# Kernel optimization log

Measured on AMD Instinct MI355X. Metric: run time of the kernel, lower is better.

Reference implementation:

```python
import jax, jax.numpy as jnp
import numpy as np

NUM_LABELS = 1000
HIDDEN = 512
BATCH = 65536
NOISE_STD = 0.1
L_STAB, L_CENTER, L_SEP, L_BRIER = 1.0, 0.1, 0.01, 1.0


def setup_inputs() -> dict:
    key = jax.random.key(0)
    k1, k2, k3, k4, k5 = jax.random.split(key, 5)
    cls_rep = jax.random.normal(k1, (BATCH, HIDDEN), dtype=jnp.float32)
    logits = jax.random.normal(k2, (BATCH, NUM_LABELS), dtype=jnp.float32)
    labels = jax.random.randint(k3, (BATCH,), 0, NUM_LABELS)
    W = jax.random.normal(k4, (HIDDEN, NUM_LABELS), dtype=jnp.float32) * 0.02
    b = jnp.zeros((NUM_LABELS,), dtype=jnp.float32)
    noise = jax.random.normal(k5, (BATCH, HIDDEN), dtype=jnp.float32)
    centers = jnp.zeros((NUM_LABELS, HIDDEN), dtype=jnp.float32)
    return {"cls_rep": cls_rep, "logits": logits, "labels": labels,
            "W": W, "b": b, "noise": noise, "centers": centers}


def _compute_all(cls_rep, logits, labels, W, b, noise, centers):
    # --- update_centers (init branch, no_grad): per-class mean via segment_sum ---
    ones = jnp.ones((cls_rep.shape[0],), dtype=cls_rep.dtype)
    counts = jax.ops.segment_sum(ones, labels, num_segments=NUM_LABELS)           # [C]
    sums = jax.ops.segment_sum(cls_rep, labels, num_segments=NUM_LABELS)          # [C, H]
    present = counts > 0
    batch_means = sums / jnp.maximum(counts, 1.0)[:, None]
    new_centers = jnp.where(present[:, None], batch_means, centers)               # [C, H]
    new_centers = jax.lax.stop_gradient(new_centers)

    # --- stability: classifier(cls_rep + noise_std * eps) vs clean logits ---
    logits_noisy = (cls_rep + NOISE_STD * noise) @ W + b                          # [B, C]
    stab = jnp.mean((logits_noisy - logits) ** 2)

    # --- center loss: gather centroids, MSE ---
    center = jnp.mean((cls_rep - new_centers[labels]) ** 2)

    # --- separation: cdist + exp, minus exp(0)*num_labels ---
    sq = jnp.sum(new_centers ** 2, axis=1)                                        # [C]
    d2 = jnp.maximum(sq[:, None] + sq[None, :] - 2.0 * new_centers @ new_centers.T, 0.0)
    dist = jnp.sqrt(d2)                                                           # [C, C]
    I = jnp.eye(NUM_LABELS, dtype=dist.dtype)
    sep = jnp.sum(jnp.exp(-dist + I)) - jnp.float32(NUM_LABELS)

    # --- brier: softmax vs one-hot ---
    probs = jax.nn.softmax(logits, axis=-1)
    one_hot = jax.nn.one_hot(labels, NUM_LABELS, dtype=logits.dtype)
    brier = jnp.mean(jnp.sum((probs - one_hot) ** 2, axis=1))

    total = L_STAB * stab + L_CENTER * center + L_SEP * sep + L_BRIER * brier
    return jnp.stack([total, stab, center, sep, brier])


def reference(cls_rep, logits, labels, W, b, noise, centers):
    return _compute_all(cls_rep, logits, labels, W, b, noise, centers)
```

## Files before the change

### kernel.cpp

```cpp
#include <hip/hip_runtime.h>

#define BATCH 65536
#define HID   512
#define NCLS  1000
#define NCLSP 1024

typedef long i64;
typedef float f32x4 __attribute__((ext_vector_type(4)));
typedef float f32x2 __attribute__((ext_vector_type(2)));
typedef unsigned short u16;
typedef unsigned int u32;
typedef unsigned char u8;

__device__ __forceinline__ u32 pk4(float a, float b, float c, float d) {
  u32 r = 0;
  r = (u32)__builtin_amdgcn_cvt_pk_fp8_f32(a, b, (int)r, false);
  r = (u32)__builtin_amdgcn_cvt_pk_fp8_f32(c, d, (int)r, true);
  return r;
}
__device__ __forceinline__ u8 pk1(float a) {
  return (u8)(__builtin_amdgcn_cvt_pk_fp8_f32(a, 0.f, 0, false) & 0xff);
}

#define WS_END 2908160

__global__ void k_zero(int* __restrict__ counts, int* __restrict__ cursor,
                       double* __restrict__ accum) {
  const int t = threadIdx.x;
  counts[t] = 0;
  cursor[t] = 0;
  if (t < 8) accum[t] = 0.0;
}

__global__ void k_hist(const int* __restrict__ labels, int* __restrict__ counts) {
  const int i = blockIdx.x * blockDim.x + threadIdx.x;
  if (i < BATCH) atomicAdd(counts + labels[i], 1);
}

__global__ void k_wconv(const float* __restrict__ W, u32* __restrict__ wb) {
  const int j = blockIdx.x * blockDim.x + threadIdx.x;
  const int kc = j >> 13, col = (j >> 3) & 1023, kg = (j >> 1) & 3, i0 = (j & 1) * 4;
  const int k = kc * 32 + kg * 8 + i0;
  float w0 = 0.f, w1 = 0.f, w2 = 0.f, w3 = 0.f;
  if (col < NCLS) {
    w0 = W[(size_t)(k + 0) * NCLS + col] * 16.f;
    w1 = W[(size_t)(k + 1) * NCLS + col] * 16.f;
    w2 = W[(size_t)(k + 2) * NCLS + col] * 16.f;
    w3 = W[(size_t)(k + 3) * NCLS + col] * 16.f;
  }
  wb[j] = pk4(w0, w1, w2, w3);
}

__global__ void k_scatter(const int* __restrict__ labels, const int* __restrict__ counts,
                          int* __restrict__ cursor, int* __restrict__ offsets,
                          int* __restrict__ order) {
  __shared__ int scan[1024];
  __shared__ int wsum[16];
  const int t = threadIdx.x;
  const int v = counts[t];
  int x = v;
  #pragma unroll
  for (int d = 1; d < 64; d <<= 1) {
    int y = __shfl_up(x, d);
    if ((t & 63) >= d) x += y;
  }
  if ((t & 63) == 63) wsum[t >> 6] = x;
  __syncthreads();
  if (t < 16) {
    int s = wsum[t];
    #pragma unroll
    for (int d = 1; d < 16; d <<= 1) {
      int y = __shfl_up(s, d);
      if (t >= d) s += y;
    }
    wsum[t] = s;
  }
  __syncthreads();
  const int base = (t >= 64) ? wsum[(t >> 6) - 1] : 0;
  const int incl = base + x;
  scan[t] = incl - v;
  if (blockIdx.x == 0) offsets[t] = incl;
  __syncthreads();
  const int i = blockIdx.x * 1024 + t;
  if (i < BATCH) {
    const int lab = labels[i];
    const int pos = scan[lab] + atomicAdd(cursor + lab, 1);
    order[pos] = i;
  }
}

__global__ void k_segsum(const float* __restrict__ cls, const int* __restrict__ order,
                         const int* __restrict__ offsets, const int* __restrict__ counts,
                         const float* __restrict__ cen_in, float* __restrict__ cen,
                         float* __restrict__ sq, double* __restrict__ accum) {
  __shared__ float red[8];
  __shared__ float redc[8];
  const int c = blockIdx.x;
  const int t = threadIdx.x;
  const int cnt = counts[c];
  const int end = offsets[c];
  const int start = end - cnt;
  float v, cp;
  if (cnt > 0) {
    float s0 = 0.f, s1 = 0.f, s2 = 0.f, s3 = 0.f;
    float q0 = 0.f, q1 = 0.f, q2 = 0.f, q3 = 0.f;
    int i = start;
    for (; i + 4 <= end; i += 4) {
      const int r0 = order[i], r1 = order[i + 1], r2 = order[i + 2], r3 = order[i + 3];
      float x0 = cls[(size_t)r0 * HID + t];
      float x1 = cls[(size_t)r1 * HID + t];
      float x2 = cls[(size_t)r2 * HID + t];
      float x3 = cls[(size_t)r3 * HID + t];
      s0 += x0; q0 = fmaf(x0, x0, q0);
      s1 += x1; q1 = fmaf(x1, x1, q1);
      s2 += x2; q2 = fmaf(x2, x2, q2);
      s3 += x3; q3 = fmaf(x3, x3, q3);
    }
    for (; i < end; ++i) {
      float x = cls[(size_t)order[i] * HID + t];
      s0 += x; q0 = fmaf(x, x, q0);
    }
    v = ((s0 + s1) + (s2 + s3)) / (float)cnt;
    cp = ((q0 + q1) + (q2 + q3)) - (float)cnt * v * v;
  } else {
    v = (c < NCLS) ? cen_in[(size_t)c * HID + t] : 0.f;
    cp = 0.f;
  }
  cen[(size_t)c * HID + t] = v;

  float p = v * v;
  #pragma unroll
  for (int s = 32; s; s >>= 1) { p += __shfl_xor(p, s); cp += __shfl_xor(cp, s); }
  if ((t & 63) == 0) { red[t >> 6] = p; redc[t >> 6] = cp; }
  __syncthreads();
  if (t == 0) {
    float acc = 0.f, accc = 0.f;
    #pragma unroll
    for (int i = 0; i < 8; ++i) { acc += red[i]; accc += redc[i]; }
    sq[c] = acc;
    atomicAdd(accum + 1, (double)accc);
  }
}

__global__ void k_sep(const float* __restrict__ cen, const float* __restrict__ sq,
                      double* __restrict__ accum) {
  __shared__ float As[16][64];
  __shared__ float Bs[16][64];
  __shared__ float red[4];
  const int bi = blockIdx.x >> 4, bj = blockIdx.x & 15;
  const int tx = threadIdx.x & 15, ty = threadIdx.x >> 4;
  const int lrow = threadIdx.x & 63, lkq = threadIdx.x >> 6;
  float acc[4][4] = {};
  for (int k0 = 0; k0 < HID; k0 += 16) {
    __syncthreads();
    float4 a = *(const float4*)(cen + (size_t)(bi * 64 + lrow) * HID + k0 + lkq * 4);
    float4 b = *(const float4*)(cen + (size_t)(bj * 64 + lrow) * HID + k0 + lkq * 4);
    As[lkq*4+0][lrow] = a.x; As[lkq*4+1][lrow] = a.y; As[lkq*4+2][lrow] = a.z; As[lkq*4+3][lrow] = a.w;
    Bs[lkq*4+0][lrow] = b.x; Bs[lkq*4+1][lrow] = b.y; Bs[lkq*4+2][lrow] = b.z; Bs[lkq*4+3][lrow] = b.w;
    __syncthreads();
    #pragma unroll
    for (int k = 0; k < 16; ++k) {
      float4 av = *(const float4*)&As[k][ty * 4];
      float4 bv = *(const float4*)&Bs[k][tx * 4];
      float ar[4] = {av.x, av.y, av.z, av.w};
      float br[4] = {bv.x, bv.y, bv.z, bv.w};
      #pragma unroll
      for (int r = 0; r < 4; ++r)
        #pragma unroll
        for (int s = 0; s < 4; ++s)
          acc[r][s] = fmaf(ar[r], br[s], acc[r][s]);
    }
  }
  float part = 0.f;
  #pragma unroll
  for (int r = 0; r < 4; ++r) {
    const int i = bi * 64 + ty * 4 + r;
    #pragma unroll
    for (int s = 0; s < 4; ++s) {
      const int j = bj * 64 + tx * 4 + s;
      if (i < NCLS && j < NCLS) {
        float d2 = fmaxf(sq[i] + sq[j] - 2.f * acc[r][s], 0.f);
        float dist = sqrtf(d2);
        part += __expf((i == j ? 1.f : 0.f) - dist);
      }
    }
  }
  #pragma unroll
  for (int s = 32; s; s >>= 1) part += __shfl_xor(part, s);
  if ((threadIdx.x & 63) == 0) red[threadIdx.x >> 6] = part;
  __syncthreads();
  if (threadIdx.x == 0)
    atomicAdd(accum + 2, (double)(red[0] + red[1] + red[2] + red[3]));
}

__global__ __launch_bounds__(1024, 8)
void k_gemm(const float* __restrict__ cls, const float* __restrict__ noise,
            const float* __restrict__ logits, const int* __restrict__ labels,
            const float* __restrict__ bias, const u8* __restrict__ wb,
            double* __restrict__ accum) {
  __shared__ u8 Apan[32 * 512];
  __shared__ u8 lntile[32 * 1024];
  __shared__ float redf[32];
  const int lane = threadIdx.x & 63;
  const int w = threadIdx.x >> 6;
  const int row0 = blockIdx.x * 32;
  const int l15 = lane & 15, lkg = lane >> 4;

  {
    const int row_loc = threadIdx.x >> 5;
    const int k0 = (threadIdx.x & 31) * 16;
    const int sw = ((row_loc & 7) << 3) | (((row_loc >> 3) & 1) << 6);
    const float* cp = cls   + (size_t)(row0 + row_loc) * HID;
    const float* np = noise + (size_t)(row0 + row_loc) * HID;
    #pragma unroll
    for (int q = 0; q < 2; ++q) {
      const int g = k0 + q * 8;
      const int k = g ^ sw;
      float4 a0 = *(const float4*)(cp + k), a1 = *(const float4*)(cp + k + 4);
      float4 n0 = *(const float4*)(np + k), n1 = *(const float4*)(np + k + 4);
      uint2 p;
      p.x = pk4(fmaf(0.1f, n0.x, a0.x), fmaf(0.1f, n0.y, a0.y),
                fmaf(0.1f, n0.z, a0.z), fmaf(0.1f, n0.w, a0.w));
      p.y = pk4(fmaf(0.1f, n1.x, a1.x), fmaf(0.1f, n1.y, a1.y),
                fmaf(0.1f, n1.z, a1.z), fmaf(0.1f, n1.w, a1.w));
      *(uint2*)&Apan[row_loc * 512 + g] = p;
    }
  }
  __syncthreads();

  f32x4 acc[2][4] = {};
  const int swr = ((l15 & 7) << 3) | ((l15 >> 3) << 6);
  const u8* bb0 = wb + (w * 64 + l15) * 32 + lkg * 8;
  i64 bcur[4];
  #pragma unroll
  for (int ct = 0; ct < 4; ++ct) bcur[ct] = *(const i64*)(bb0 + ct * 512);
  for (int kc = 0; kc < 16; ++kc) {
    const int kn = (kc < 15) ? kc + 1 : 15;
    const u8* bbn = bb0 + (size_t)kn * 32768;
    i64 bnxt[4];
    #pragma unroll
    for (int ct = 0; ct < 4; ++ct) bnxt[ct] = *(const i64*)(bbn + ct * 512);
    i64 af0 = *(const i64*)&Apan[(l15)      * 512 + ((kc * 32 + lkg * 8) ^ swr)];
    i64 af1 = *(const i64*)&Apan[(16 + l15) * 512 + ((kc * 32 + lkg * 8) ^ swr)];
    #pragma unroll
    for (int ct = 0; ct < 4; ++ct) {
      acc[0][ct] = __builtin_amdgcn_mfma_f32_16x16x32_fp8_fp8(af0, bcur[ct], acc[0][ct], 0, 0, 0);
      acc[1][ct] = __builtin_amdgcn_mfma_f32_16x16x32_fp8_fp8(af1, bcur[ct], acc[1][ct], 0, 0, 0);
    }
    #pragma unroll
    for (int ct = 0; ct < 4; ++ct) bcur[ct] = bnxt[ct];
  }

  #pragma unroll
  for (int ct = 0; ct < 4; ++ct) {
    const int col = w * 64 + ct * 16 + l15;
    if (col < NCLS) {
      const float bc = bias[col];
      #pragma unroll
      for (int rt = 0; rt < 2; ++rt) {
        #pragma unroll
        for (int r = 0; r < 4; ++r) {
          const int rowloc = rt * 16 + lkg * 4 + r;
          lntile[rowloc * 1024 + (col ^ ((rowloc & 12) << 2))] =
              pk1(fmaf(acc[rt][ct][r], 0.0625f, bc));
        }
      }
    }
  }
  __syncthreads();

  float spart = 0.f, bpart = 0.f;
  #pragma unroll
  for (int j = 0; j < 2; ++j) {
    const int rowloc = w * 2 + j;
    const int row = row0 + rowloc;
    const int swz = (rowloc & 12) << 2;
    const u8* lnrow = lntile + rowloc * 1024;
    const float4* lr = (const float4*)(logits + (size_t)row * NCLS);
    const int lab2 = labels[row];
    const float el = __expf(logits[(size_t)row * NCLS + lab2]);
    float S = 0.f, S2 = 0.f;
    #pragma unroll
    for (int it = 0; it < 4; ++it) {
      const int f = it * 64 + lane;
      if (f < 250) {
        float4 lg = lr[f];
        u32 v = *(const u32*)(lnrow + ((f * 4) ^ swz));
        f32x2 lo = __builtin_amdgcn_cvt_pk_f32_fp8((int)v, false);
        f32x2 hi = __builtin_amdgcn_cvt_pk_f32_fp8((int)v, true);
        float d0 = lo[0] - lg.x, d1 = lo[1] - lg.y, d2 = hi[0] - lg.z, d3 = hi[1] - lg.w;
        spart += d0 * d0 + d1 * d1 + d2 * d2 + d3 * d3;
        float e0 = __expf(lg.x), e1 = __expf(lg.y), e2 = __expf(lg.z), e3 = __expf(lg.w);
        S += e0 + e1 + e2 + e3;
        S2 += e0 * e0 + e1 * e1 + e2 * e2 + e3 * e3;
      }
    }
    #pragma unroll
    for (int s = 32; s; s >>= 1) { S += __shfl_xor(S, s); S2 += __shfl_xor(S2, s); }
    bpart += S2 / (S * S) - 2.f * el / S + 1.f;
  }
  #pragma unroll
  for (int s = 32; s; s >>= 1) { spart += __shfl_xor(spart, s); bpart += __shfl_xor(bpart, s); }

  if (lane == 0) { redf[w] = spart; redf[16 + w] = bpart; }
  __syncthreads();
  if (threadIdx.x == 0) {
    float st = 0.f, br = 0.f;
    #pragma unroll
    for (int i = 0; i < 16; ++i) { st += redf[i]; br += redf[16 + i]; }
    atomicAdd(accum + 0, (double)st);
    atomicAdd(accum + 3, (double)br);
  }
}

__global__ void k_final(const double* __restrict__ accum, float* __restrict__ out) {
  if (threadIdx.x == 0) {
    double stab   = accum[0] / ((double)BATCH * (double)NCLS);
    double center = accum[1] / ((double)BATCH * (double)HID);
    double sep    = accum[2] - (double)NCLS;
    double brier  = accum[3] / (double)BATCH;
    double total  = 1.0 * stab + 0.1 * center + 0.01 * sep + 1.0 * brier;
    out[0] = (float)total;
    out[1] = (float)stab;
    out[2] = (float)center;
    out[3] = (float)sep;
    out[4] = (float)brier;
  }
}

extern "C" void kernel_launch(void* const* d_in, const int* in_sizes, int n_in,
                              void* d_out, int out_size, void* d_ws, size_t ws_size,
                              hipStream_t stream) {
  const float* cls    = (const float*)d_in[0];
  const float* logits = (const float*)d_in[1];
  const int*   labels = (const int*)d_in[2];
  const float* W      = (const float*)d_in[3];
  const float* bias   = (const float*)d_in[4];
  const float* noise  = (const float*)d_in[5];
  const float* cen_in = (const float*)d_in[6];
  float* out = (float*)d_out;
  char* ws = (char*)d_ws;
  if (ws_size < (size_t)WS_END) return;

  int*    counts  = (int*)(ws + 0);
  int*    cursor  = (int*)(ws + 4096);
  double* accum   = (double*)(ws + 8192);
  float*  sq      = (float*)(ws + 12288);
  int*    offsets = (int*)(ws + 16384);
  int*    order   = (int*)(ws + 20480);
  float*  cen     = (float*)(ws + 282624);
  u8*     wb8     = (u8*)(ws + 2383872);

  hipLaunchKernelGGL(k_zero,    dim3(1),    dim3(1024), 0, stream, counts, cursor, accum);
  hipLaunchKernelGGL(k_hist,    dim3(256),  dim3(256),  0, stream, labels, counts);
  hipLaunchKernelGGL(k_wconv,   dim3(512),  dim3(256),  0, stream, W, (u32*)wb8);
  hipLaunchKernelGGL(k_scatter, dim3(64),   dim3(1024), 0, stream, labels, counts, cursor, offsets, order);
  hipLaunchKernelGGL(k_segsum,  dim3(1024), dim3(512),  0, stream, cls, order, offsets, counts, cen_in, cen, sq, accum);
  hipLaunchKernelGGL(k_sep,     dim3(256),  dim3(256),  0, stream, cen, sq, accum);
  hipLaunchKernelGGL(k_gemm,    dim3(2048), dim3(1024), 0, stream, cls, noise, logits, labels, bias, wb8, accum);
  hipLaunchKernelGGL(k_final,   dim3(1),    dim3(64),   0, stream, accum, out);
}
```

Measured before the change: 254.9 us.

## Use symmetric upper-triangle 32x32 tiles in separation kernel for more parallelism

The pairwise-distance kernel now uses 32x32 output tiles over a 32x32 grid, with 4 outputs per thread instead of 16. Blocks below the diagonal exit early and off-diagonal contributions are doubled, exploiting symmetry of the distance matrix. Shared-memory tiles are padded to 33 columns to reduce bank conflicts. This trades lower per-thread register reuse and more launched blocks for better occupancy on a small, latency-bound kernel.

```diff
diff --git a/kernel.cpp b/kernel.cpp
--- a/kernel.cpp
+++ b/kernel.cpp
@@ -142,54 +142,58 @@
   }
 }
 
-__global__ void k_sep(const float* __restrict__ cen, const float* __restrict__ sq,
-                      double* __restrict__ accum) {
-  __shared__ float As[16][64];
-  __shared__ float Bs[16][64];
+__global__ __launch_bounds__(256)
+void k_sep(const float* __restrict__ cen, const float* __restrict__ sq,
+           double* __restrict__ accum) {
+  const int bi = blockIdx.x >> 5, bj = blockIdx.x & 31;
+  if (bj < bi) return;
+  __shared__ float As[16][33];
+  __shared__ float Bs[16][33];
   __shared__ float red[4];
-  const int bi = blockIdx.x >> 4, bj = blockIdx.x & 15;
-  const int tx = threadIdx.x & 15, ty = threadIdx.x >> 4;
-  const int lrow = threadIdx.x & 63, lkq = threadIdx.x >> 6;
-  float acc[4][4] = {};
+  const int t = threadIdx.x;
+  const int ty = t >> 3;
+  const int tx4 = (t & 7) * 4;
+  float acc[4] = {};
   for (int k0 = 0; k0 < HID; k0 += 16) {
     __syncthreads();
-    float4 a = *(const float4*)(cen + (size_t)(bi * 64 + lrow) * HID + k0 + lkq * 4);
-    float4 b = *(const float4*)(cen + (size_t)(bj * 64 + lrow) * HID + k0 + lkq * 4);
-    As[lkq*4+0][lrow] = a.x; As[lkq*4+1][lrow] = a.y; As[lkq*4+2][lrow] = a.z; As[lkq*4+3][lrow] = a.w;
-    Bs[lkq*4+0][lrow] = b.x; Bs[lkq*4+1][lrow] = b.y; Bs[lkq*4+2][lrow] = b.z; Bs[lkq*4+3][lrow] = b.w;
+    {
+      const int c = (t & 127) >> 2;
+      const int kq = (t & 3) * 4;
+      const int row = ((t < 128) ? bi : bj) * 32 + c;
+      float4 v = *(const float4*)(cen + (size_t)row * HID + k0 + kq);
+      float (*buf)[33] = (t < 128) ? As : Bs;
+      buf[kq + 0][c] = v.x;
+      buf[kq + 1][c] = v.y;
+      buf[kq + 2][c] = v.z;
+      buf[kq + 3][c] = v.w;
+    }
     __syncthreads();
     #pragma unroll
     for (int k = 0; k < 16; ++k) {
-      float4 av = *(const float4*)&As[k][ty * 4];
-      float4 bv = *(const float4*)&Bs[k][tx * 4];
-      float ar[4] = {av.x, av.y, av.z, av.w};
-      float br[4] = {bv.x, bv.y, bv.z, bv.w};
-      #pragma unroll
-      for (int r = 0; r < 4; ++r)
-        #pragma unroll
-        for (int s = 0; s < 4; ++s)
-          acc[r][s] = fmaf(ar[r], br[s], acc[r][s]);
+      const float a = As[k][ty];
+      const float4 b = *(const float4*)&Bs[k][tx4];
+      acc[0] = fmaf(a, b.x, acc[0]);
+      acc[1] = fmaf(a, b.y, acc[1]);
+      acc[2] = fmaf(a, b.z, acc[2]);
+      acc[3] = fmaf(a, b.w, acc[3]);
     }
   }
   float part = 0.f;
-  #pragma unroll
-  for (int r = 0; r < 4; ++r) {
-    const int i = bi * 64 + ty * 4 + r;
-    #pragma unroll
-    for (int s = 0; s < 4; ++s) {
-      const int j = bj * 64 + tx * 4 + s;
-      if (i < NCLS && j < NCLS) {
-        float d2 = fmaxf(sq[i] + sq[j] - 2.f * acc[r][s], 0.f);
-        float dist = sqrtf(d2);
-        part += __expf((i == j ? 1.f : 0.f) - dist);
-      }
-    }
-  }
-  #pragma unroll
-  for (int s = 32; s; s >>= 1) part += __shfl_xor(part, s);
-  if ((threadIdx.x & 63) == 0) red[threadIdx.x >> 6] = part;
-  __syncthreads();
-  if (threadIdx.x == 0)
+  const int i = bi * 32 + ty;
+  #pragma unroll
+  for (int s2 = 0; s2 < 4; ++s2) {
+    const int j = bj * 32 + tx4 + s2;
+    if (i < NCLS && j < NCLS) {
+      float d2 = fmaxf(sq[i] + sq[j] - 2.f * acc[s2], 0.f);
+      part += __expf((i == j ? 1.f : 0.f) - sqrtf(d2));
+    }
+  }
+  if (bi != bj) part *= 2.f;
+  #pragma unroll
+  for (int sh = 32; sh; sh >>= 1) part += __shfl_xor(part, sh);
+  if ((t & 63) == 0) red[t >> 6] = part;
+  __syncthreads();
+  if (t == 0)
     atomicAdd(accum + 2, (double)(red[0] + red[1] + red[2] + red[3]));
 }
 
@@ -356,7 +360,7 @@
   hipLaunchKernelGGL(k_wconv,   dim3(512),  dim3(256),  0, stream, W, (u32*)wb8);
   hipLaunchKernelGGL(k_scatter, dim3(64),   dim3(1024), 0, stream, labels, counts, cursor, offsets, order);
   hipLaunchKernelGGL(k_segsum,  dim3(1024), dim3(512),  0, stream, cls, order, offsets, counts, cen_in, cen, sq, accum);
-  hipLaunchKernelGGL(k_sep,     dim3(256),  dim3(256),  0, stream, cen, sq, accum);
+  hipLaunchKernelGGL(k_sep,     dim3(1024), dim3(256),  0, stream, cen, sq, accum);
   hipLaunchKernelGGL(k_gemm,    dim3(2048), dim3(1024), 0, stream, cls, noise, logits, labels, bias, wb8, accum);
   hipLaunchKernelGGL(k_final,   dim3(1),    dim3(64),   0, stream, accum, out);
 }
```

Measured after the change: 262.4 us. +2.9%, slower.
